# Optimization experiments

Hardware: AMD Instinct MI355X
Metric: run time of the kernel (lower is better)

Reference implementation:

```python
import jax, jax.numpy as jnp
import numpy as np

N_NODES = 20000
N_EDGES = 160000
IN_DIM = 2048
HID = 512


def setup_inputs() -> dict:
    key = jax.random.key(0)
    ks = jax.random.split(key, 12)
    s1 = 1.0 / np.sqrt(IN_DIM)
    s2 = 1.0 / np.sqrt(HID)
    return {
        "x": jax.random.normal(ks[0], (N_NODES, IN_DIM), dtype=jnp.float32),
        "edge_index": jax.random.randint(ks[1], (2, N_EDGES), 0, N_NODES, dtype=jnp.int64),
        "W1": jax.random.uniform(ks[2], (IN_DIM, HID), jnp.float32, -s1, s1),
        "b1": jax.random.uniform(ks[3], (HID,), jnp.float32, -s1, s1),
        "W2": jax.random.uniform(ks[4], (HID, HID), jnp.float32, -s2, s2),
        "b2": jax.random.uniform(ks[5], (HID,), jnp.float32, -s2, s2),
        "Wg": jax.random.uniform(ks[6], (HID, HID), jnp.float32, -s2, s2),
        "bg": jax.random.uniform(ks[7], (HID,), jnp.float32, -s2, s2),
        "Wa": jax.random.uniform(ks[8], (HID, 1), jnp.float32, -s2, s2),
        "ba": jax.random.uniform(ks[9], (1,), jnp.float32, -s2, s2),
    }


def reference(x, edge_index, W1, b1, W2, b2, Wg, bg, Wa, ba):
    # GINConv (eps=0): h = MLP((1+eps)*x + sum_{j in N(i)} x_j)
    src, dst = edge_index[0], edge_index[1]
    agg = jax.ops.segment_sum(x[src], dst, num_segments=x.shape[0])  # [N, IN_DIM]
    h = x + agg
    h = jnp.maximum(h @ W1 + b1, 0.0) @ W2 + b2  # [N, HID]
    # Gated attention pooling scores
    A = jnp.tanh(h @ Wg + bg)                    # [N, HID]
    alpha = (A @ Wa + ba)[:, 0]                  # [N]
    att_scores = jax.nn.softmax(alpha, axis=0)   # softmax over all nodes
    return (h, att_scores)
```

## Files before the change

kernel.cpp:

```cpp
#include <hip/hip_runtime.h>

typedef __attribute__((ext_vector_type(8))) __bf16 bf16x8;
typedef __attribute__((ext_vector_type(4))) __bf16 bf16x4;
typedef __attribute__((ext_vector_type(4))) float f32x4;
typedef __attribute__((ext_vector_type(8))) unsigned short u16x8;

__device__ __forceinline__ bf16x8 cvt8(float4 a, float4 b) {
    bf16x8 o;
    o[0] = (__bf16)a.x; o[1] = (__bf16)a.y; o[2] = (__bf16)a.z; o[3] = (__bf16)a.w;
    o[4] = (__bf16)b.x; o[5] = (__bf16)b.y; o[6] = (__bf16)b.z; o[7] = (__bf16)b.w;
    return o;
}
__device__ __forceinline__ bf16x4 cvt4(f32x4 v) {
    bf16x4 o;
    o[0] = (__bf16)v[0]; o[1] = (__bf16)v[1]; o[2] = (__bf16)v[2]; o[3] = (__bf16)v[3];
    return o;
}

__device__ __forceinline__ unsigned swz(int row, int s) {
    return (unsigned)((row * 64 + s * 16) ^ ((row & 8) << 2));
}

__global__ __launch_bounds__(256) void convw_pre_kernel(const float* __restrict__ W,
                                                        char* __restrict__ out, int K) {
    int t = blockIdx.x * 256 + threadIdx.x;
    if (t >= K * 512) return;
    int k = t >> 9, n = t & 511;
    int cb = n >> 8, r = n & 255, tt = k >> 5, s = (k & 31) >> 3, e = k & 7;
    size_t off = ((size_t)cb * (K >> 5) + tt) * 16384 + swz(r, s) + e * 2;
    *(__bf16*)(out + off) = (__bf16)W[t];
}

__global__ __launch_bounds__(256) void count_kernel(const int* __restrict__ dst,
                                                    int* __restrict__ counts, int E) {
    int e = blockIdx.x * 256 + threadIdx.x;
    if (e < E) atomicAdd(&counts[dst[e]], 1);
}

__global__ __launch_bounds__(1024) void scan_kernel(const int* __restrict__ counts,
                                                    int* __restrict__ offs, int N) {
    __shared__ int wsum[16], wpre[16];
    const int CH = 20;
    int tid = threadIdx.x, lane = tid & 63, wv = tid >> 6;
    int base = tid * CH;
    int s = 0;
    for (int i = 0; i < CH; i++) { int idx = base + i; s += (idx < N) ? counts[idx] : 0; }
    int run = s;
#pragma unroll
    for (int o = 1; o < 64; o <<= 1) { int v = __shfl_up(run, o, 64); if (lane >= o) run += v; }
    if (lane == 63) wsum[wv] = run;
    __syncthreads();
    if (tid == 0) { int acc = 0; for (int w = 0; w < 16; w++) { wpre[w] = acc; acc += wsum[w]; } }
    __syncthreads();
    int pre = wpre[wv] + (run - s);
    for (int i = 0; i < CH; i++) {
        int idx = base + i;
        if (idx <= N) offs[idx] = pre;
        pre += (idx < N) ? counts[idx] : 0;
    }
}

__global__ __launch_bounds__(256) void bucket_kernel(const int* __restrict__ src,
                                                     const int* __restrict__ dst,
                                                     const int* __restrict__ offs,
                                                     int* __restrict__ cursor,
                                                     int* __restrict__ eids, int E) {
    int e = blockIdx.x * 256 + threadIdx.x;
    if (e >= E) return;
    int d = dst[e];
    int pos = atomicAdd(&cursor[d], 1);
    eids[offs[d] + pos] = src[e];
}

__global__ __launch_bounds__(256) void addy4_kernel(const __bf16* __restrict__ p,
                                                    __bf16* __restrict__ y) {
    size_t i = ((size_t)blockIdx.x * 256 + threadIdx.x) * 8;
    bf16x8 a = *(const bf16x8*)(p + i);
    bf16x8 b = *(const bf16x8*)(p + 10240000 + i);
    bf16x8 c = *(const bf16x8*)(p + 20480000 + i);
    bf16x8 d = *(const bf16x8*)(p + 30720000 + i);
    bf16x8 o;
#pragma unroll
    for (int j = 0; j < 8; j++)
        o[j] = (__bf16)(((float)a[j] + (float)b[j]) + ((float)c[j] + (float)d[j]));
    *(bf16x8*)(y + i) = o;
}

__global__ __launch_bounds__(256) void gather_h1_kernel(const __bf16* __restrict__ y,
                                                        const int* __restrict__ offs,
                                                        const int* __restrict__ eids,
                                                        const float* __restrict__ b1,
                                                        __bf16* __restrict__ h1b) {
    const int node = blockIdx.x * 4 + (threadIdx.x >> 6);
    const int c = (threadIdx.x & 63) * 8;
    float s[8];
    bf16x8 v = *(const bf16x8*)(y + (size_t)node * 512 + c);
#pragma unroll
    for (int j = 0; j < 8; j++) s[j] = (float)v[j];
    const int beg = offs[node], end = offs[node + 1];
    for (int k = beg; k < end; k++) {
        int sn = eids[k];
        bf16x8 u = *(const bf16x8*)(y + (size_t)sn * 512 + c);
#pragma unroll
        for (int j = 0; j < 8; j++) s[j] += (float)u[j];
    }
    bf16x8 o;
#pragma unroll
    for (int j = 0; j < 8; j++) o[j] = (__bf16)fmaxf(s[j] + b1[c + j], 0.f);
    *(bf16x8*)(h1b + (size_t)node * 512 + c) = o;
}

__global__ __launch_bounds__(512, 4) void gemm1_kernel(const float* __restrict__ X,
                                                       const char* __restrict__ Bpre,
                                                       __bf16* __restrict__ Ybase, int M) {
    extern __shared__ char smem[];
    const int tid = threadIdx.x, lane = tid & 63, wv = tid >> 6;
    const int fr = lane & 15, sec = lane >> 4, hi4 = (lane >> 4) * 4;
    const long row0 = (long)blockIdx.x * 64;
    const int kh = blockIdx.y;
    const int cb = wv >> 2, rbase = (wv & 3) * 64;
    const char* Bp = Bpre + ((size_t)cb * 64 + (size_t)kh * 16) * 16384;
    __bf16* Y = Ybase + (size_t)kh * 10240000;

#pragma unroll
    for (int j = 0; j < 8; j++) {
        int b = tid * 16 + j * 8192;
        int tt = b >> 12, bb = b & 4095;
        int row = bb >> 6, soff = bb & 63;
        int s = (soff ^ ((row & 8) << 2)) >> 4;
        long arow = row0 + row; if (arow > (long)M - 1) arow = M - 1;
        const float* p = X + arow * 2048 + kh * 512 + tt * 32 + s * 8;
        float4 a0 = *(const float4*)p;
        float4 a1 = *(const float4*)(p + 4);
        *(bf16x8*)(smem + b) = cvt8(a0, a1);
    }
    __syncthreads();

    f32x4 acc[4][4];
#pragma unroll
    for (int m = 0; m < 4; m++)
#pragma unroll
        for (int n = 0; n < 4; n++)
#pragma unroll
            for (int r = 0; r < 4; r++) acc[m][n][r] = 0.f;

    for (int tt = 0; tt < 16; tt++) {
        const char* at = smem + tt * 4096;
        const char* bt = Bp + (size_t)tt * 16384;
        bf16x8 wf[4], xf[4];
#pragma unroll
        for (int m = 0; m < 4; m++)
            wf[m] = *(const bf16x8*)(bt + swz(rbase + m * 16 + fr, sec));
#pragma unroll
        for (int n = 0; n < 4; n++)
            xf[n] = *(const bf16x8*)(at + swz(n * 16 + fr, sec));
#pragma unroll
        for (int m = 0; m < 4; m++)
#pragma unroll
            for (int n = 0; n < 4; n++)
                acc[m][n] = __builtin_amdgcn_mfma_f32_16x16x32_bf16(wf[m], xf[n], acc[m][n], 0, 0, 0);
    }

#pragma unroll
    for (int n = 0; n < 4; n++) {
        long node = row0 + n * 16 + fr;
        if (node < M) {
#pragma unroll
            for (int m = 0; m < 4; m++) {
                int col = cb * 256 + rbase + m * 16 + hi4;
                *(bf16x4*)(Y + node * 512 + col) = cvt4(acc[m][n]);
            }
        }
    }
}

__global__ __launch_bounds__(512) void mlp23_kernel(const __bf16* __restrict__ H1,
                                                    const char* __restrict__ W2p,
                                                    const float* __restrict__ b2,
                                                    const char* __restrict__ Wgp,
                                                    const float* __restrict__ bg,
                                                    const float* __restrict__ Wa,
                                                    float* __restrict__ Hout,
                                                    float* __restrict__ alpha) {
    constexpr int NT2 = 8;
    __shared__ char smem[41216];
    char* Hs = smem + 8192;
    float* aS = (float*)(smem + 40960);
    const int tid = threadIdx.x, lane = tid & 63, wv = tid >> 6;
    const int fr = lane & 15, sec = lane >> 4, hi4 = (lane >> 4) * 4;
    const long row0 = (long)blockIdx.x * 32;
    const int cbv = wv >> 2, rbase = (wv & 3) * 64;

    if (tid < 32) aS[tid] = 0.f;

    const int b16 = tid * 16;
    const int sh = b16 >> 11;
    const int bb = b16 & 2047;
    const int srow = bb >> 6;
    const int soff = bb & 63;
    const int ss = (soff ^ ((srow & 8) << 2)) >> 4;
    const __bf16* ApH = H1 + (row0 + srow) * 512 + sh * 32 + ss * 8;

#define ASEC(b) (smem + (b) * 4096)

    f32x4 acc[4][2];
#pragma unroll
    for (int m = 0; m < 4; m++)
#pragma unroll
        for (int n = 0; n < 2; n++)
#pragma unroll
            for (int r = 0; r < 4; r++) acc[m][n][r] = 0.f;

    if (tid < 256) {
        u16x8 v = *(const u16x8*)(ApH);
        *(u16x8*)(ASEC(0) + b16) = v;
    }
    asm volatile("s_waitcnt lgkmcnt(0)" ::: "memory");
    __builtin_amdgcn_s_barrier();

    int cur = 0;
    for (int tt = 0; tt < NT2; tt++) {
        u16x8 av;
        const bool more = (tt + 1 < NT2);
        if (more && tid < 256) av = *(const u16x8*)(ApH + (tt + 1) * 64);
#pragma unroll
        for (int h = 0; h < 2; h++) {
            const char* bt = W2p + ((size_t)cbv * 16 + tt * 2 + h) * 16384;
            bf16x8 wf[4], xf[2];
#pragma unroll
            for (int m = 0; m < 4; m++)
                wf[m] = *(const bf16x8*)(bt + swz(rbase + m * 16 + fr, sec));
#pragma unroll
            for (int n = 0; n < 2; n++)
                xf[n] = *(const bf16x8*)(ASEC(cur) + h * 2048 + swz(n * 16 + fr, sec));
#pragma unroll
            for (int m = 0; m < 4; m++)
#pragma unroll
                for (int n = 0; n < 2; n++)
                    acc[m][n] = __builtin_amdgcn_mfma_f32_16x16x32_bf16(wf[m], xf[n], acc[m][n], 0, 0, 0);
        }
        if (more) {
            const int nxt = cur ^ 1;
            if (tid < 256) *(u16x8*)(ASEC(nxt) + b16) = av;
            asm volatile("s_waitcnt lgkmcnt(0)" ::: "memory");
            __builtin_amdgcn_s_barrier();
            cur = nxt;
        }
    }

#pragma unroll
    for (int n = 0; n < 2; n++) {
        int node = n * 16 + fr;
        long gnode = row0 + node;
#pragma unroll
        for (int m = 0; m < 4; m++) {
            int hc = wv * 64 + m * 16 + hi4;
            f32x4 bv = *(const f32x4*)(b2 + hc);
            f32x4 v = acc[m][n] + bv;
            *(f32x4*)(Hout + gnode * 512 + hc) = v;
            int tt = hc >> 5, sk = (hc & 31) >> 3, e = hc & 7;
            *(bf16x4*)(Hs + tt * 2048 + swz(node, sk) + e * 2) = cvt4(v);
        }
    }
    asm volatile("s_waitcnt lgkmcnt(0)" ::: "memory");
    __builtin_amdgcn_s_barrier();

    f32x4 acc2[4][2];
#pragma unroll
    for (int m = 0; m < 4; m++)
#pragma unroll
        for (int n = 0; n < 2; n++)
#pragma unroll
            for (int r = 0; r < 4; r++) acc2[m][n][r] = 0.f;

    for (int g = 0; g < 16; g++) {
        const char* bt = Wgp + ((size_t)cbv * 16 + g) * 16384;
        bf16x8 wf[4], xf[2];
#pragma unroll
        for (int m = 0; m < 4; m++)
            wf[m] = *(const bf16x8*)(bt + swz(rbase + m * 16 + fr, sec));
#pragma unroll
        for (int n = 0; n < 2; n++)
            xf[n] = *(const bf16x8*)(Hs + g * 2048 + swz(n * 16 + fr, sec));
#pragma unroll
        for (int m = 0; m < 4; m++)
#pragma unroll
            for (int n = 0; n < 2; n++)
                acc2[m][n] = __builtin_amdgcn_mfma_f32_16x16x32_bf16(wf[m], xf[n], acc2[m][n], 0, 0, 0);
    }
#undef ASEC

#pragma unroll
    for (int n = 0; n < 2; n++) {
        float s = 0.f;
#pragma unroll
        for (int m = 0; m < 4; m++) {
            int gc = wv * 64 + m * 16 + hi4;
            f32x4 bgv = *(const f32x4*)(bg + gc);
            f32x4 wav = *(const f32x4*)(Wa + gc);
#pragma unroll
            for (int r = 0; r < 4; r++)
                s += tanhf(acc2[m][n][r] + bgv[r]) * wav[r];
        }
        s += __shfl_xor(s, 16, 64);
        s += __shfl_xor(s, 32, 64);
        if (sec == 0) atomicAdd(&aS[n * 16 + fr], s);
    }
    __syncthreads();
    if (tid < 32) alpha[row0 + tid] = aS[tid];
}

__global__ __launch_bounds__(1024) void softmax_kernel(const float* __restrict__ alpha,
                                                       float* __restrict__ att, int N) {
    __shared__ float red[16];
    __shared__ float bc[2];
    int tid = threadIdx.x, lane = tid & 63, wv = tid >> 6;
    float m = -3.4e38f;
    for (int i = tid; i < N; i += 1024) m = fmaxf(m, alpha[i]);
#pragma unroll
    for (int o = 32; o > 0; o >>= 1) m = fmaxf(m, __shfl_xor(m, o, 64));
    if (lane == 0) red[wv] = m;
    __syncthreads();
    if (tid == 0) {
        float mm = red[0];
        for (int i = 1; i < 16; i++) mm = fmaxf(mm, red[i]);
        bc[0] = mm;
    }
    __syncthreads();
    float Mx = bc[0];
    float s = 0.f;
    for (int i = tid; i < N; i += 1024) s += expf(alpha[i] - Mx);
#pragma unroll
    for (int o = 32; o > 0; o >>= 1) s += __shfl_xor(s, o, 64);
    if (lane == 0) red[wv] = s;
    __syncthreads();
    if (tid == 0) {
        float ss = 0.f;
        for (int i = 0; i < 16; i++) ss += red[i];
        bc[1] = ss;
    }
    __syncthreads();
    float inv = 1.f / bc[1];
    for (int i = tid; i < N; i += 1024) att[i] = expf(alpha[i] - Mx) * inv;
}

extern "C" void kernel_launch(void* const* d_in, const int* in_sizes, int n_in,
                              void* d_out, int out_size, void* d_ws, size_t ws_size,
                              hipStream_t stream) {
    const float* x  = (const float*)d_in[0];
    const int*   ei = (const int*)d_in[1];
    const float* W1 = (const float*)d_in[2];
    const float* b1 = (const float*)d_in[3];
    const float* W2 = (const float*)d_in[4];
    const float* b2 = (const float*)d_in[5];
    const float* Wg = (const float*)d_in[6];
    const float* bg = (const float*)d_in[7];
    const float* Wa = (const float*)d_in[8];

    const int M = 20000, IN = 2048, H = 512, E = 160000;

    char* ws = (char*)d_ws;
    __bf16* yp    = (__bf16*)ws;
    __bf16* ysum  = (__bf16*)(ws + 81920000);
    char*  W1p    = ws + 102400000;
    char*  W2p    = ws + 104497152;
    char*  Wgp    = ws + 105021440;
    __bf16* h1b   = (__bf16*)(ws + 105545728);
    float* alpha  = (float*)(ws + 126025728);
    int*   counts = (int*)(ws + 126105728);
    int*   offs   = (int*)(ws + 126185728);
    int*   cursor = (int*)(ws + 126265732);
    int*   eids   = (int*)(ws + 126345732);

    float* hout = (float*)d_out;
    float* att  = hout + (size_t)M * H;

    convw_pre_kernel<<<4096, 256, 0, stream>>>(W1, W1p, IN);
    convw_pre_kernel<<<1024, 256, 0, stream>>>(W2, W2p, H);
    convw_pre_kernel<<<1024, 256, 0, stream>>>(Wg, Wgp, H);

    hipMemsetAsync(counts, 0, M * 4, stream);
    count_kernel<<<(E + 255) / 256, 256, 0, stream>>>(ei + E, counts, E);
    scan_kernel<<<1, 1024, 0, stream>>>(counts, offs, M);
    hipMemsetAsync(cursor, 0, M * 4, stream);
    bucket_kernel<<<(E + 255) / 256, 256, 0, stream>>>(ei, ei + E, offs, cursor, eids, E);

    gemm1_kernel<<<dim3(313, 4), 512, 65536, stream>>>(x, W1p, yp, M);
    addy4_kernel<<<5000, 256, 0, stream>>>(yp, ysum);

    gather_h1_kernel<<<5000, 256, 0, stream>>>(ysum, offs, eids, b1, h1b);

    mlp23_kernel<<<625, 512, 0, stream>>>(h1b, W2p, b2, Wgp, bg, Wa, hout, alpha);

    softmax_kernel<<<1, 1024, 0, stream>>>(alpha, att, M);
}
```

Baseline: 288.4 us.

## Double-buffer W1 fragment loads and enlarge mlp23 row tile to 64

```diff
diff --git a/kernel.cpp b/kernel.cpp
--- a/kernel.cpp
+++ b/kernel.cpp
@@ -122,6 +122,15 @@
     const char* Bp = Bpre + ((size_t)cb * 64 + (size_t)kh * 16) * 16384;
     __bf16* Y = Ybase + (size_t)kh * 10240000;
 
+#define LOAD_WF(dst, g) do {                                              \
+        const char* bt_ = Bp + (size_t)(g) * 16384;                       \
+        _Pragma("unroll") for (int m_ = 0; m_ < 4; m_++)                  \
+            dst[m_] = *(const bf16x8*)(bt_ + swz(rbase + m_ * 16 + fr, sec)); \
+    } while (0)
+
+    bf16x8 wfA[4], wfB[4];
+    LOAD_WF(wfA, 0);
+
 #pragma unroll
     for (int j = 0; j < 8; j++) {
         int b = tid * 16 + j * 8192;
@@ -144,22 +153,25 @@
 #pragma unroll
             for (int r = 0; r < 4; r++) acc[m][n][r] = 0.f;
 
-    for (int tt = 0; tt < 16; tt++) {
-        const char* at = smem + tt * 4096;
-        const char* bt = Bp + (size_t)tt * 16384;
-        bf16x8 wf[4], xf[4];
-#pragma unroll
-        for (int m = 0; m < 4; m++)
-            wf[m] = *(const bf16x8*)(bt + swz(rbase + m * 16 + fr, sec));
-#pragma unroll
-        for (int n = 0; n < 4; n++)
-            xf[n] = *(const bf16x8*)(at + swz(n * 16 + fr, sec));
-#pragma unroll
-        for (int m = 0; m < 4; m++)
-#pragma unroll
-            for (int n = 0; n < 4; n++)
-                acc[m][n] = __builtin_amdgcn_mfma_f32_16x16x32_bf16(wf[m], xf[n], acc[m][n], 0, 0, 0);
-    }
+#define COMPUTE(t, wf) do {                                               \
+        const char* at_ = smem + (t) * 4096;                              \
+        bf16x8 xf[4];                                                     \
+        _Pragma("unroll") for (int n_ = 0; n_ < 4; n_++)                  \
+            xf[n_] = *(const bf16x8*)(at_ + swz(n_ * 16 + fr, sec));      \
+        _Pragma("unroll") for (int m_ = 0; m_ < 4; m_++)                  \
+            _Pragma("unroll") for (int n_ = 0; n_ < 4; n_++)              \
+                acc[m_][n_] = __builtin_amdgcn_mfma_f32_16x16x32_bf16(    \
+                    wf[m_], xf[n_], acc[m_][n_], 0, 0, 0);                \
+    } while (0)
+
+    for (int tt = 0; tt < 16; tt += 2) {
+        LOAD_WF(wfB, tt + 1);
+        COMPUTE(tt, wfA);
+        if (tt + 2 < 16) LOAD_WF(wfA, tt + 2);
+        COMPUTE(tt + 1, wfB);
+    }
+#undef COMPUTE
+#undef LOAD_WF
 
 #pragma unroll
     for (int n = 0; n < 4; n++) {
@@ -181,37 +193,36 @@
                                                     const float* __restrict__ bg,
                                                     const float* __restrict__ Wa,
                                                     float* __restrict__ Hout,
-                                                    float* __restrict__ alpha) {
-    constexpr int NT2 = 8;
-    __shared__ char smem[41216];
-    char* Hs = smem + 8192;
-    float* aS = (float*)(smem + 40960);
+                                                    float* __restrict__ alpha, int M) {
+    __shared__ char smem[81920];
+    char* Hs = smem + 16384;
+    float* aS = (float*)smem;
     const int tid = threadIdx.x, lane = tid & 63, wv = tid >> 6;
     const int fr = lane & 15, sec = lane >> 4, hi4 = (lane >> 4) * 4;
-    const long row0 = (long)blockIdx.x * 32;
-    const int cbv = wv >> 2, rbase = (wv & 3) * 64;
-
-    if (tid < 32) aS[tid] = 0.f;
+    const long row0 = (long)blockIdx.x * 64;
+    const int wm = wv >> 2, wn = wv & 3;
+    const int cbv = wn >> 1, rbase = (wn & 1) * 128;
 
     const int b16 = tid * 16;
-    const int sh = b16 >> 11;
-    const int bb = b16 & 2047;
+    const int sh = b16 >> 12;
+    const int bb = b16 & 4095;
     const int srow = bb >> 6;
     const int soff = bb & 63;
     const int ss = (soff ^ ((srow & 8) << 2)) >> 4;
-    const __bf16* ApH = H1 + (row0 + srow) * 512 + sh * 32 + ss * 8;
-
-#define ASEC(b) (smem + (b) * 4096)
-
-    f32x4 acc[4][2];
-#pragma unroll
-    for (int m = 0; m < 4; m++)
+    long arow = row0 + srow; if (arow > (long)M - 1) arow = M - 1;
+    const __bf16* ApH = H1 + arow * 512 + sh * 32 + ss * 8;
+
+#define ASEC(b) (smem + (b) * 8192)
+
+    f32x4 acc[8][2];
+#pragma unroll
+    for (int m = 0; m < 8; m++)
 #pragma unroll
         for (int n = 0; n < 2; n++)
 #pragma unroll
             for (int r = 0; r < 4; r++) acc[m][n][r] = 0.f;
 
-    if (tid < 256) {
+    {
         u16x8 v = *(const u16x8*)(ApH);
         *(u16x8*)(ASEC(0) + b16) = v;
     }
@@ -219,29 +230,29 @@
     __builtin_amdgcn_s_barrier();
 
     int cur = 0;
-    for (int tt = 0; tt < NT2; tt++) {
+    for (int tt = 0; tt < 8; tt++) {
         u16x8 av;
-        const bool more = (tt + 1 < NT2);
-        if (more && tid < 256) av = *(const u16x8*)(ApH + (tt + 1) * 64);
+        const bool more = (tt + 1 < 8);
+        if (more) av = *(const u16x8*)(ApH + (tt + 1) * 64);
 #pragma unroll
         for (int h = 0; h < 2; h++) {
             const char* bt = W2p + ((size_t)cbv * 16 + tt * 2 + h) * 16384;
-            bf16x8 wf[4], xf[2];
-#pragma unroll
-            for (int m = 0; m < 4; m++)
+            bf16x8 wf[8], xf[2];
+#pragma unroll
+            for (int m = 0; m < 8; m++)
                 wf[m] = *(const bf16x8*)(bt + swz(rbase + m * 16 + fr, sec));
 #pragma unroll
             for (int n = 0; n < 2; n++)
-                xf[n] = *(const bf16x8*)(ASEC(cur) + h * 2048 + swz(n * 16 + fr, sec));
-#pragma unroll
-            for (int m = 0; m < 4; m++)
+                xf[n] = *(const bf16x8*)(ASEC(cur) + h * 4096 + swz(wm * 32 + n * 16 + fr, sec));
+#pragma unroll
+            for (int m = 0; m < 8; m++)
 #pragma unroll
                 for (int n = 0; n < 2; n++)
                     acc[m][n] = __builtin_amdgcn_mfma_f32_16x16x32_bf16(wf[m], xf[n], acc[m][n], 0, 0, 0);
         }
         if (more) {
             const int nxt = cur ^ 1;
-            if (tid < 256) *(u16x8*)(ASEC(nxt) + b16) = av;
+            *(u16x8*)(ASEC(nxt) + b16) = av;
             asm volatile("s_waitcnt lgkmcnt(0)" ::: "memory");
             __builtin_amdgcn_s_barrier();
             cur = nxt;
@@ -250,24 +261,25 @@
 
 #pragma unroll
     for (int n = 0; n < 2; n++) {
-        int node = n * 16 + fr;
+        int node = wm * 32 + n * 16 + fr;
         long gnode = row0 + node;
 #pragma unroll
-        for (int m = 0; m < 4; m++) {
-            int hc = wv * 64 + m * 16 + hi4;
+        for (int m = 0; m < 8; m++) {
+            int hc = wn * 128 + m * 16 + hi4;
             f32x4 bv = *(const f32x4*)(b2 + hc);
             f32x4 v = acc[m][n] + bv;
-            *(f32x4*)(Hout + gnode * 512 + hc) = v;
+            if (gnode < M) *(f32x4*)(Hout + gnode * 512 + hc) = v;
             int tt = hc >> 5, sk = (hc & 31) >> 3, e = hc & 7;
-            *(bf16x4*)(Hs + tt * 2048 + swz(node, sk) + e * 2) = cvt4(v);
+            *(bf16x4*)(Hs + tt * 4096 + swz(node, sk) + e * 2) = cvt4(v);
         }
     }
+    if (tid < 64) aS[tid] = 0.f;
     asm volatile("s_waitcnt lgkmcnt(0)" ::: "memory");
     __builtin_amdgcn_s_barrier();
 
-    f32x4 acc2[4][2];
-#pragma unroll
-    for (int m = 0; m < 4; m++)
+    f32x4 acc2[8][2];
+#pragma unroll
+    for (int m = 0; m < 8; m++)
 #pragma unroll
         for (int n = 0; n < 2; n++)
 #pragma unroll
@@ -275,15 +287,15 @@
 
     for (int g = 0; g < 16; g++) {
         const char* bt = Wgp + ((size_t)cbv * 16 + g) * 16384;
-        bf16x8 wf[4], xf[2];
-#pragma unroll
-        for (int m = 0; m < 4; m++)
+        bf16x8 wf[8], xf[2];
+#pragma unroll
+        for (int m = 0; m < 8; m++)
             wf[m] = *(const bf16x8*)(bt + swz(rbase + m * 16 + fr, sec));
 #pragma unroll
         for (int n = 0; n < 2; n++)
-            xf[n] = *(const bf16x8*)(Hs + g * 2048 + swz(n * 16 + fr, sec));
-#pragma unroll
-        for (int m = 0; m < 4; m++)
+            xf[n] = *(const bf16x8*)(Hs + g * 4096 + swz(wm * 32 + n * 16 + fr, sec));
+#pragma unroll
+        for (int m = 0; m < 8; m++)
 #pragma unroll
             for (int n = 0; n < 2; n++)
                 acc2[m][n] = __builtin_amdgcn_mfma_f32_16x16x32_bf16(wf[m], xf[n], acc2[m][n], 0, 0, 0);
@@ -294,8 +306,8 @@
     for (int n = 0; n < 2; n++) {
         float s = 0.f;
 #pragma unroll
-        for (int m = 0; m < 4; m++) {
-            int gc = wv * 64 + m * 16 + hi4;
+        for (int m = 0; m < 8; m++) {
+            int gc = wn * 128 + m * 16 + hi4;
             f32x4 bgv = *(const f32x4*)(bg + gc);
             f32x4 wav = *(const f32x4*)(Wa + gc);
 #pragma unroll
@@ -304,10 +316,13 @@
         }
         s += __shfl_xor(s, 16, 64);
         s += __shfl_xor(s, 32, 64);
-        if (sec == 0) atomicAdd(&aS[n * 16 + fr], s);
-    }
-    __syncthreads();
-    if (tid < 32) alpha[row0 + tid] = aS[tid];
+        if (sec == 0) atomicAdd(&aS[wm * 32 + n * 16 + fr], s);
+    }
+    __syncthreads();
+    if (tid < 64) {
+        long node = row0 + tid;
+        if (node < M) alpha[node] = aS[tid];
+    }
 }
 
 __global__ __launch_bounds__(1024) void softmax_kernel(const float* __restrict__ alpha,
@@ -390,7 +405,7 @@
 
     gather_h1_kernel<<<5000, 256, 0, stream>>>(ysum, offs, eids, b1, h1b);
 
-    mlp23_kernel<<<625, 512, 0, stream>>>(h1b, W2p, b2, Wgp, bg, Wa, hout, alpha);
+    mlp23_kernel<<<313, 512, 0, stream>>>(h1b, W2p, b2, Wgp, bg, Wa, hout, alpha, M);
 
     softmax_kernel<<<1, 1024, 0, stream>>>(alpha, att, M);
 }
```

Result: slower. 324.5 us (+12.5%).
